# Performance work log

Measured on AMD Instinct MI355X. Metric: run time of the kernel, lower is better.

The kernel has to match this reference:

```python
import jax, jax.numpy as jnp
import numpy as np

B, S, D_MODEL, D_KEY = 4, 2048, 1024, 128


def setup_inputs() -> dict:
    key = jax.random.key(0)
    kq, kk, kv, kwq, kwk, kwv = jax.random.split(key, 6)
    queries = jax.random.normal(kq, (B, S, D_MODEL), dtype=jnp.float32)
    keys = jax.random.normal(kk, (B, S, D_MODEL), dtype=jnp.float32)
    values = jax.random.normal(kv, (B, S, D_MODEL), dtype=jnp.float32)
    # causal mask: 1 where attention is allowed (j <= i), 0 otherwise
    mask = jnp.broadcast_to(jnp.tril(jnp.ones((S, S), dtype=jnp.int32)), (B, S, S))
    # torch nn.Linear weights are [out, in]; init ~ U(-1/sqrt(in), 1/sqrt(in))
    bound = 1.0 / np.sqrt(D_MODEL)
    Wq = jax.random.uniform(kwq, (D_KEY, D_MODEL), jnp.float32, -bound, bound)
    Wk = jax.random.uniform(kwk, (D_KEY, D_MODEL), jnp.float32, -bound, bound)
    Wv = jax.random.uniform(kwv, (D_KEY, D_MODEL), jnp.float32, -bound, bound)
    return {"queries": queries, "keys": keys, "values": values, "mask": mask,
            "Wq": Wq, "Wk": Wk, "Wv": Wv}


def reference(queries, keys, values, mask, Wq, Wk, Wv):
    d_key = Wq.shape[0]
    q = jnp.einsum('bsd,kd->bsk', queries, Wq)   # [B,S,d_key]
    k = jnp.einsum('bsd,kd->bsk', keys, Wk)
    v = jnp.einsum('bsd,kd->bsk', values, Wv)
    attn = jnp.einsum('bqk,bsk->bqs', q, k) / jnp.sqrt(jnp.float32(d_key))  # [B,S,S]
    attn = jnp.where(mask == 0, -jnp.inf, attn)
    attn = jax.nn.softmax(attn, axis=-1)
    return jnp.einsum('bqs,bsk->bqk', attn, v)   # [B,S,d_key]
```

## Files before the change

### kernel.cpp

```cpp
#include <hip/hip_runtime.h>
#include <hip/hip_bf16.h>

#define NB 4
#define SEQ 2048
#define DMODEL 1024
#define DKEY 128

using f32x4  = __attribute__((ext_vector_type(4))) float;
using bf16x8 = __attribute__((ext_vector_type(8))) short;
using u16x4  = __attribute__((ext_vector_type(4))) unsigned short;
using u16x8  = __attribute__((ext_vector_type(8))) unsigned short;

__device__ __forceinline__ unsigned short f2bf(float f) {
  __hip_bfloat16 h = __float2bfloat16(f);
  return __builtin_bit_cast(unsigned short, h);
}
__device__ __forceinline__ void gload16(const void* g, void* l) {
  __builtin_amdgcn_global_load_lds(
      (const __attribute__((address_space(1))) void*)g,
      (__attribute__((address_space(3))) void*)l, 16, 0, 0);
}

__global__ __launch_bounds__(256) void proj_kernel(
    const float* __restrict__ Xq, const float* __restrict__ Xk, const float* __restrict__ Xv,
    const float* __restrict__ Wq, const float* __restrict__ Wk, const float* __restrict__ Wv,
    unsigned short* __restrict__ Yq, unsigned short* __restrict__ Yk,
    unsigned short* __restrict__ Vt)
{
  const int z = blockIdx.z;
  const float* X = (z == 0) ? Xq : (z == 1) ? Xk : Xv;
  const float* W = (z == 0) ? Wq : (z == 1) ? Wk : Wv;

  __shared__ alignas(16) unsigned short Xl[2][64][40];
  __shared__ alignas(16) unsigned short Wl[2][128][40];
  __shared__ alignas(16) unsigned short Tl[128][72];

  const int t     = threadIdx.x;
  const int lane  = t & 63;
  const int w     = t >> 6;
  const int lr    = lane & 15;
  const int lk    = (lane >> 4) * 8;
  const int rbase = (lane >> 4) * 4;
  const long m0   = (long)blockIdx.x * 64;

  f32x4 acc[8];
  const f32x4 zero = {0.f, 0.f, 0.f, 0.f};
#pragma unroll
  for (int n = 0; n < 8; ++n) acc[n] = zero;

  float4 xr[2], wr[4];
#pragma unroll
  for (int i = 0; i < 2; ++i) {
    int id = t + 256 * i, row = id >> 3, c4 = (id & 7) << 2;
    xr[i] = *reinterpret_cast<const float4*>(&X[(m0 + row) * DMODEL + c4]);
  }
#pragma unroll
  for (int i = 0; i < 4; ++i) {
    int id = t + 256 * i, row = id >> 3, c4 = (id & 7) << 2;
    wr[i] = *reinterpret_cast<const float4*>(&W[(long)row * DMODEL + c4]);
  }

  for (int ks = 0; ks < DMODEL / 32; ++ks) {
    const int cur = ks & 1;
#pragma unroll
    for (int i = 0; i < 2; ++i) {
      int id = t + 256 * i, row = id >> 3, c4 = (id & 7) << 2;
      u16x4 p = { f2bf(xr[i].x), f2bf(xr[i].y), f2bf(xr[i].z), f2bf(xr[i].w) };
      *reinterpret_cast<u16x4*>(&Xl[cur][row][c4]) = p;
    }
#pragma unroll
    for (int i = 0; i < 4; ++i) {
      int id = t + 256 * i, row = id >> 3, c4 = (id & 7) << 2;
      u16x4 p = { f2bf(wr[i].x), f2bf(wr[i].y), f2bf(wr[i].z), f2bf(wr[i].w) };
      *reinterpret_cast<u16x4*>(&Wl[cur][row][c4]) = p;
    }
    if (ks + 1 < DMODEL / 32) {
      const int k0 = (ks + 1) * 32;
#pragma unroll
      for (int i = 0; i < 2; ++i) {
        int id = t + 256 * i, row = id >> 3, c4 = (id & 7) << 2;
        xr[i] = *reinterpret_cast<const float4*>(&X[(m0 + row) * DMODEL + k0 + c4]);
      }
#pragma unroll
      for (int i = 0; i < 4; ++i) {
        int id = t + 256 * i, row = id >> 3, c4 = (id & 7) << 2;
        wr[i] = *reinterpret_cast<const float4*>(&W[(long)row * DMODEL + k0 + c4]);
      }
    }
    __syncthreads();

    bf16x8 a = *reinterpret_cast<const bf16x8*>(&Xl[cur][w * 16 + lr][lk]);
#pragma unroll
    for (int n = 0; n < 8; ++n) {
      bf16x8 b = *reinterpret_cast<const bf16x8*>(&Wl[cur][n * 16 + lr][lk]);
      acc[n] = __builtin_amdgcn_mfma_f32_16x16x32_bf16(a, b, acc[n], 0, 0, 0);
    }
  }

  if (z != 2) {
    unsigned short* Y = (z == 0) ? Yq : Yk;
#pragma unroll
    for (int n = 0; n < 8; ++n)
#pragma unroll
      for (int r = 0; r < 4; ++r) {
        long row = m0 + w * 16 + rbase + r;
        Y[row * DKEY + n * 16 + lr] = f2bf(acc[n][r]);
      }
  } else {
#pragma unroll
    for (int n = 0; n < 8; ++n)
#pragma unroll
      for (int r = 0; r < 4; ++r)
        Tl[n * 16 + lr][w * 16 + rbase + r] = f2bf(acc[n][r]);
    __syncthreads();
    const int bb = (int)(m0 >> 11);
    const int s0 = (int)(m0 & 2047);
#pragma unroll
    for (int i = 0; i < 4; ++i) {
      int id = t + 256 * i;
      int dr = id >> 3;
      int c8 = (id & 7) << 3;
      u16x8 v = *reinterpret_cast<const u16x8*>(&Tl[dr][c8]);
      *reinterpret_cast<u16x8*>(&Vt[((size_t)bb * DKEY + dr) * SEQ + s0 + c8]) = v;
    }
  }
}

__global__ __launch_bounds__(512, 2) void attn_kernel(
    const unsigned short* __restrict__ Q,
    const unsigned short* __restrict__ K,
    const unsigned short* __restrict__ Vt,
    float* __restrict__ O)
{
  const int  L    = blockIdx.x;
  const int  b    = (L & 7) >> 1;
  const int  qt   = 63 - (((L >> 3) << 1) | (L & 1));
  const int  q0   = qt * 32;
  const long base = (long)b * SEQ;
  const int  nt   = (q0 >> 6) + 1;
  const int  nsteps = (nt + 3) >> 2;

  __shared__ alignas(16) unsigned short Kl[4][64][128];
  __shared__ alignas(16) unsigned short Vl[4][128][64];
  __shared__ alignas(16) unsigned short Plds[8][16][72];
  __shared__ float Sm[4][32], Sl[4][32];

  const int t     = threadIdx.x;
  const int lane  = t & 63;
  const int w     = t >> 6;
  const int g     = w >> 1;
  const int wq    = w & 1;
  const int lr    = lane & 15;
  const int hi    = lane >> 4;
  const int lk    = hi * 8;
  const int rbase = hi * 4;

  bf16x8 qa[4];
  {
    const long qrow = (base + q0 + wq * 16 + lr) * (long)DKEY;
#pragma unroll
    for (int dk = 0; dk < 4; ++dk)
      qa[dk] = *reinterpret_cast<const bf16x8*>(&Q[qrow + dk * 32 + lk]);
  }

  const f32x4 zero = {0.f, 0.f, 0.f, 0.f};
  f32x4 oacc[8];
#pragma unroll
  for (int n = 0; n < 8; ++n) oacc[n] = zero;
  float m_run[4], l_run[4];
#pragma unroll
  for (int r = 0; r < 4; ++r) { m_run[r] = -1e30f; l_run[r] = 0.0f; }

  const float sc = 0.08838834764831845f;
  const unsigned short* VtB = Vt + (size_t)b * DKEY * SEQ;

  for (int st = 0; st < nsteps; ++st) {
    const int kt  = st * 4 + g;
    const bool act = kt < nt;
    const int kv0 = kt * 64;

    if (act) {
      const unsigned short* Kp = K + (base + kv0) * (long)DKEY;
      char* Kd = (char*)(&Kl[g][0][0]);
#pragma unroll
      for (int it = 0; it < 8; ++it) {
        int c = it * 128 + wq * 64 + lane;
        int row = c >> 4, d = c & 15;
        int srcg = (c & ~15) | (d ^ (row & 7));
        gload16(&Kp[(size_t)srcg * 8], Kd + (size_t)c * 16);
      }
      char* Vd = (char*)(&Vl[g][0][0]);
#pragma unroll
      for (int it = 0; it < 8; ++it) {
        int c = it * 128 + wq * 64 + lane;
        int drow = c >> 3, sl = c & 7;
        int srcc = (sl ^ (drow & 7)) << 3;
        gload16(&VtB[(size_t)drow * SEQ + kv0 + srcc], Vd + (size_t)c * 16);
      }
    }
    __syncthreads();

    if (act) {
      f32x4 s[4];
#pragma unroll
      for (int kc = 0; kc < 4; ++kc) {
        s[kc] = zero;
#pragma unroll
        for (int dk = 0; dk < 4; ++dk) {
          bf16x8 kb = *reinterpret_cast<const bf16x8*>(
              &Kl[g][kc * 16 + lr][((dk * 4 + hi) ^ (lr & 7)) * 8]);
          s[kc] = __builtin_amdgcn_mfma_f32_16x16x32_bf16(qa[dk], kb, s[kc], 0, 0, 0);
        }
      }

      const bool dmask = (kt == nt - 1);
      float x[4][4];
#pragma unroll
      for (int kc = 0; kc < 4; ++kc)
#pragma unroll
        for (int r = 0; r < 4; ++r) {
          float xv = s[kc][r] * sc;
          if (dmask) {
            int col  = kv0 + kc * 16 + lr;
            int rowq = q0 + wq * 16 + rbase + r;
            if (col > rowq) xv = -1e30f;
          }
          x[kc][r] = xv;
        }

#pragma unroll
      for (int r = 0; r < 4; ++r) {
        float tm = fmaxf(fmaxf(x[0][r], x[1][r]), fmaxf(x[2][r], x[3][r]));
        tm = fmaxf(tm, __shfl_xor(tm, 1));
        tm = fmaxf(tm, __shfl_xor(tm, 2));
        tm = fmaxf(tm, __shfl_xor(tm, 4));
        tm = fmaxf(tm, __shfl_xor(tm, 8));
        float mnew = fmaxf(m_run[r], tm);
        float scl  = __expf(m_run[r] - mnew);
        m_run[r] = mnew;
        float ps = 0.0f;
#pragma unroll
        for (int kc = 0; kc < 4; ++kc) {
          float pp = __expf(x[kc][r] - mnew);
          ps += pp;
          Plds[w][rbase + r][kc * 16 + lr] = f2bf(pp);
        }
        ps += __shfl_xor(ps, 1);
        ps += __shfl_xor(ps, 2);
        ps += __shfl_xor(ps, 4);
        ps += __shfl_xor(ps, 8);
        l_run[r] = l_run[r] * scl + ps;
#pragma unroll
        for (int n = 0; n < 8; ++n) oacc[n][r] *= scl;
      }

#pragma unroll
      for (int kk = 0; kk < 2; ++kk) {
        bf16x8 pa = *reinterpret_cast<const bf16x8*>(&Plds[w][lr][kk * 32 + lk]);
#pragma unroll
        for (int n = 0; n < 8; ++n) {
          bf16x8 vb = *reinterpret_cast<const bf16x8*>(
              &Vl[g][n * 16 + lr][((kk * 4 + hi) ^ (lr & 7)) * 8]);
          oacc[n] = __builtin_amdgcn_mfma_f32_16x16x32_bf16(pa, vb, oacc[n], 0, 0, 0);
        }
      }
    }
    __syncthreads();
  }

  float* Om = reinterpret_cast<float*>(&Kl[0][0][0]);
#pragma unroll
  for (int n = 0; n < 8; ++n)
#pragma unroll
    for (int r = 0; r < 4; ++r)
      Om[(g * 32 + wq * 16 + rbase + r) * 128 + n * 16 + lr] = oacc[n][r];
  if (lr == 0) {
#pragma unroll
    for (int r = 0; r < 4; ++r) {
      Sm[g][wq * 16 + rbase + r] = m_run[r];
      Sl[g][wq * 16 + rbase + r] = l_run[r];
    }
  }
  __syncthreads();

  const int row = t >> 4;
  const int c0  = (t & 15) * 8;
  float mM = fmaxf(fmaxf(Sm[0][row], Sm[1][row]), fmaxf(Sm[2][row], Sm[3][row]));
  float wts[4], lsum = 0.0f;
#pragma unroll
  for (int gv = 0; gv < 4; ++gv) {
    wts[gv] = __expf(Sm[gv][row] - mM);
    lsum += wts[gv] * Sl[gv][row];
  }
  const float linv = 1.0f / lsum;
  f32x4 o0 = zero, o1 = zero;
#pragma unroll
  for (int gv = 0; gv < 4; ++gv) {
    const float* src = &Om[(gv * 32 + row) * 128 + c0];
    f32x4 a0 = *reinterpret_cast<const f32x4*>(src);
    f32x4 a1 = *reinterpret_cast<const f32x4*>(src + 4);
    const float wt = wts[gv];
#pragma unroll
    for (int j = 0; j < 4; ++j) { o0[j] += wt * a0[j]; o1[j] += wt * a1[j]; }
  }
#pragma unroll
  for (int j = 0; j < 4; ++j) { o0[j] *= linv; o1[j] *= linv; }
  float* op = &O[(base + q0 + row) * (long)DKEY + c0];
  *reinterpret_cast<f32x4*>(op)     = o0;
  *reinterpret_cast<f32x4*>(op + 4) = o1;
}

extern "C" void kernel_launch(void* const* d_in, const int* in_sizes, int n_in,
                              void* d_out, int out_size, void* d_ws, size_t ws_size,
                              hipStream_t stream) {
  const float* Xq = (const float*)d_in[0];
  const float* Xk = (const float*)d_in[1];
  const float* Xv = (const float*)d_in[2];
  const float* Wq = (const float*)d_in[4];
  const float* Wk = (const float*)d_in[5];
  const float* Wv = (const float*)d_in[6];

  unsigned short* qp  = (unsigned short*)d_ws;
  unsigned short* kp  = qp + (size_t)NB * SEQ * DKEY;
  unsigned short* vtp = kp + (size_t)NB * SEQ * DKEY;

  dim3 g1(SEQ * NB / 64, 1, 3);
  hipLaunchKernelGGL(proj_kernel, g1, dim3(256), 0, stream,
                     Xq, Xk, Xv, Wq, Wk, Wv, qp, kp, vtp);
  hipLaunchKernelGGL(attn_kernel, dim3(256), dim3(512), 0, stream,
                     qp, kp, vtp, (float*)d_out);
}
```

Measured before the change: 58.67 us.

## Pre-convert weights to bf16 and double projection M-tile to 128 rows

Adds a small kernel that converts Wq/Wk/Wv to bf16 once, staging them in the output buffer before attention overwrites it. The projection kernel then loads bf16 weights directly instead of converting fp32 weights in every block. Its M tile doubles to 128 rows, with two MFMA accumulator sets per wave, so each weight tile is reused across twice as many rows. This costs an extra kernel launch, more registers and LDS, and half as many blocks in the projection grid.

```diff
diff --git a/kernel.cpp b/kernel.cpp
--- a/kernel.cpp
+++ b/kernel.cpp
@@ -21,19 +21,33 @@
       (__attribute__((address_space(3))) void*)l, 16, 0, 0);
 }
 
+__global__ __launch_bounds__(256) void wconv_kernel(
+    const float* __restrict__ Wq, const float* __restrict__ Wk,
+    const float* __restrict__ Wv, unsigned short* __restrict__ Wb)
+{
+  int id = blockIdx.x * 256 + threadIdx.x;
+  const float* src = (id < 16384) ? Wq : (id < 32768) ? Wk : Wv;
+  int off = (id & 16383) * 8;
+  float4 a = *reinterpret_cast<const float4*>(&src[off]);
+  float4 b = *reinterpret_cast<const float4*>(&src[off + 4]);
+  u16x8 p = { f2bf(a.x), f2bf(a.y), f2bf(a.z), f2bf(a.w),
+              f2bf(b.x), f2bf(b.y), f2bf(b.z), f2bf(b.w) };
+  *reinterpret_cast<u16x8*>(&Wb[(size_t)(id >> 14) * 131072 + off]) = p;
+}
+
 __global__ __launch_bounds__(256) void proj_kernel(
     const float* __restrict__ Xq, const float* __restrict__ Xk, const float* __restrict__ Xv,
-    const float* __restrict__ Wq, const float* __restrict__ Wk, const float* __restrict__ Wv,
+    const unsigned short* __restrict__ Wb,
     unsigned short* __restrict__ Yq, unsigned short* __restrict__ Yk,
     unsigned short* __restrict__ Vt)
 {
   const int z = blockIdx.z;
   const float* X = (z == 0) ? Xq : (z == 1) ? Xk : Xv;
-  const float* W = (z == 0) ? Wq : (z == 1) ? Wk : Wv;
-
-  __shared__ alignas(16) unsigned short Xl[2][64][40];
+  const unsigned short* W = Wb + (size_t)z * 131072;
+
+  __shared__ alignas(16) unsigned short Xl[2][128][40];
   __shared__ alignas(16) unsigned short Wl[2][128][40];
-  __shared__ alignas(16) unsigned short Tl[128][72];
+  __shared__ alignas(16) unsigned short Tl[128][136];
 
   const int t     = threadIdx.x;
   const int lane  = t & 63;
@@ -41,85 +55,94 @@
   const int lr    = lane & 15;
   const int lk    = (lane >> 4) * 8;
   const int rbase = (lane >> 4) * 4;
-  const long m0   = (long)blockIdx.x * 64;
-
-  f32x4 acc[8];
+  const long m0   = (long)blockIdx.x * 128;
+
+  f32x4 acc[2][8];
   const f32x4 zero = {0.f, 0.f, 0.f, 0.f};
 #pragma unroll
-  for (int n = 0; n < 8; ++n) acc[n] = zero;
-
-  float4 xr[2], wr[4];
-#pragma unroll
-  for (int i = 0; i < 2; ++i) {
+  for (int m = 0; m < 2; ++m)
+#pragma unroll
+    for (int n = 0; n < 8; ++n) acc[m][n] = zero;
+
+  float4 xr[4];
+  u16x8  wr[2];
+#pragma unroll
+  for (int i = 0; i < 4; ++i) {
     int id = t + 256 * i, row = id >> 3, c4 = (id & 7) << 2;
     xr[i] = *reinterpret_cast<const float4*>(&X[(m0 + row) * DMODEL + c4]);
   }
 #pragma unroll
-  for (int i = 0; i < 4; ++i) {
-    int id = t + 256 * i, row = id >> 3, c4 = (id & 7) << 2;
-    wr[i] = *reinterpret_cast<const float4*>(&W[(long)row * DMODEL + c4]);
+  for (int i = 0; i < 2; ++i) {
+    int id = t + 256 * i, row = id >> 2, c8 = (id & 3) << 3;
+    wr[i] = *reinterpret_cast<const u16x8*>(&W[(size_t)row * DMODEL + c8]);
   }
 
   for (int ks = 0; ks < DMODEL / 32; ++ks) {
     const int cur = ks & 1;
 #pragma unroll
-    for (int i = 0; i < 2; ++i) {
+    for (int i = 0; i < 4; ++i) {
       int id = t + 256 * i, row = id >> 3, c4 = (id & 7) << 2;
       u16x4 p = { f2bf(xr[i].x), f2bf(xr[i].y), f2bf(xr[i].z), f2bf(xr[i].w) };
       *reinterpret_cast<u16x4*>(&Xl[cur][row][c4]) = p;
     }
 #pragma unroll
-    for (int i = 0; i < 4; ++i) {
-      int id = t + 256 * i, row = id >> 3, c4 = (id & 7) << 2;
-      u16x4 p = { f2bf(wr[i].x), f2bf(wr[i].y), f2bf(wr[i].z), f2bf(wr[i].w) };
-      *reinterpret_cast<u16x4*>(&Wl[cur][row][c4]) = p;
+    for (int i = 0; i < 2; ++i) {
+      int id = t + 256 * i, row = id >> 2, c8 = (id & 3) << 3;
+      *reinterpret_cast<u16x8*>(&Wl[cur][row][c8]) = wr[i];
     }
     if (ks + 1 < DMODEL / 32) {
       const int k0 = (ks + 1) * 32;
 #pragma unroll
-      for (int i = 0; i < 2; ++i) {
+      for (int i = 0; i < 4; ++i) {
         int id = t + 256 * i, row = id >> 3, c4 = (id & 7) << 2;
         xr[i] = *reinterpret_cast<const float4*>(&X[(m0 + row) * DMODEL + k0 + c4]);
       }
 #pragma unroll
-      for (int i = 0; i < 4; ++i) {
-        int id = t + 256 * i, row = id >> 3, c4 = (id & 7) << 2;
-        wr[i] = *reinterpret_cast<const float4*>(&W[(long)row * DMODEL + k0 + c4]);
-      }
-    }
-    __syncthreads();
-
-    bf16x8 a = *reinterpret_cast<const bf16x8*>(&Xl[cur][w * 16 + lr][lk]);
+      for (int i = 0; i < 2; ++i) {
+        int id = t + 256 * i, row = id >> 2, c8 = (id & 3) << 3;
+        wr[i] = *reinterpret_cast<const u16x8*>(&W[(size_t)row * DMODEL + k0 + c8]);
+      }
+    }
+    __syncthreads();
+
+    bf16x8 a0 = *reinterpret_cast<const bf16x8*>(&Xl[cur][w * 32 + lr][lk]);
+    bf16x8 a1 = *reinterpret_cast<const bf16x8*>(&Xl[cur][w * 32 + 16 + lr][lk]);
 #pragma unroll
     for (int n = 0; n < 8; ++n) {
       bf16x8 b = *reinterpret_cast<const bf16x8*>(&Wl[cur][n * 16 + lr][lk]);
-      acc[n] = __builtin_amdgcn_mfma_f32_16x16x32_bf16(a, b, acc[n], 0, 0, 0);
+      acc[0][n] = __builtin_amdgcn_mfma_f32_16x16x32_bf16(a0, b, acc[0][n], 0, 0, 0);
+      acc[1][n] = __builtin_amdgcn_mfma_f32_16x16x32_bf16(a1, b, acc[1][n], 0, 0, 0);
     }
   }
 
   if (z != 2) {
     unsigned short* Y = (z == 0) ? Yq : Yk;
 #pragma unroll
-    for (int n = 0; n < 8; ++n)
-#pragma unroll
-      for (int r = 0; r < 4; ++r) {
-        long row = m0 + w * 16 + rbase + r;
-        Y[row * DKEY + n * 16 + lr] = f2bf(acc[n][r]);
-      }
+    for (int m = 0; m < 2; ++m)
+#pragma unroll
+      for (int n = 0; n < 8; ++n)
+#pragma unroll
+        for (int r = 0; r < 4; ++r) {
+          long row = m0 + w * 32 + m * 16 + rbase + r;
+          Y[row * DKEY + n * 16 + lr] = f2bf(acc[m][n][r]);
+        }
   } else {
-#pragma unroll
-    for (int n = 0; n < 8; ++n)
-#pragma unroll
-      for (int r = 0; r < 4; ++r)
-        Tl[n * 16 + lr][w * 16 + rbase + r] = f2bf(acc[n][r]);
+    __syncthreads();
+#pragma unroll
+    for (int m = 0; m < 2; ++m)
+#pragma unroll
+      for (int n = 0; n < 8; ++n)
+#pragma unroll
+        for (int r = 0; r < 4; ++r)
+          Tl[n * 16 + lr][w * 32 + m * 16 + rbase + r] = f2bf(acc[m][n][r]);
     __syncthreads();
     const int bb = (int)(m0 >> 11);
     const int s0 = (int)(m0 & 2047);
 #pragma unroll
-    for (int i = 0; i < 4; ++i) {
+    for (int i = 0; i < 8; ++i) {
       int id = t + 256 * i;
-      int dr = id >> 3;
-      int c8 = (id & 7) << 3;
+      int dr = id >> 4;
+      int c8 = (id & 15) << 3;
       u16x8 v = *reinterpret_cast<const u16x8*>(&Tl[dr][c8]);
       *reinterpret_cast<u16x8*>(&Vt[((size_t)bb * DKEY + dr) * SEQ + s0 + c8]) = v;
     }
@@ -323,10 +346,13 @@
   unsigned short* qp  = (unsigned short*)d_ws;
   unsigned short* kp  = qp + (size_t)NB * SEQ * DKEY;
   unsigned short* vtp = kp + (size_t)NB * SEQ * DKEY;
-
-  dim3 g1(SEQ * NB / 64, 1, 3);
+  unsigned short* wbp = (unsigned short*)d_out;
+
+  hipLaunchKernelGGL(wconv_kernel, dim3(192), dim3(256), 0, stream,
+                     Wq, Wk, Wv, wbp);
+  dim3 g1(SEQ * NB / 128, 1, 3);
   hipLaunchKernelGGL(proj_kernel, g1, dim3(256), 0, stream,
-                     Xq, Xk, Xv, Wq, Wk, Wv, qp, kp, vtp);
+                     Xq, Xk, Xv, wbp, qp, kp, vtp);
   hipLaunchKernelGGL(attn_kernel, dim3(256), dim3(512), 0, stream,
                      qp, kp, vtp, (float*)d_out);
 }
```

Result: slower. 62.18 us (+6.0%).
